# Performance work log

Hardware: AMD Instinct MI355X
Metric: run time of the kernel (lower is better)

The kernel has to match this reference:

```python
import jax, jax.numpy as jnp
import numpy as np

EPS = 1e-5
HEADS = 16
DIM_HEAD = 64
ROPE_THETA = 10000.0


def layer_norm(x, g, b):
    mu = x.mean(-1, keepdims=True)
    var = x.var(-1, keepdims=True)
    return (x - mu) / jnp.sqrt(var + EPS) * g + b


def apply_rope(t):
    # t: [b, h, n, d]; interleaved-pair RoPE (rotary-embedding-torch default)
    n, d = t.shape[-2], t.shape[-1]
    inv_freq = 1.0 / (ROPE_THETA ** (jnp.arange(0, d, 2, dtype=jnp.float32) / d))  # [d/2]
    freqs = jnp.arange(n, dtype=jnp.float32)[:, None] * inv_freq[None, :]          # [n, d/2]
    freqs = jnp.repeat(freqs, 2, axis=-1)                                          # [n, d]
    cos, sin = jnp.cos(freqs).astype(t.dtype), jnp.sin(freqs).astype(t.dtype)
    t2 = t.reshape(*t.shape[:-1], d // 2, 2)
    t_rot = jnp.stack((-t2[..., 1], t2[..., 0]), axis=-1).reshape(t.shape)
    return t * cos + t_rot * sin


def setup_inputs() -> dict:
    key = jax.random.key(0)
    k0, k1, k2 = jax.random.split(key, 3)
    B, N, D = 1, 4096, 1024
    inner = HEADS * DIM_HEAD
    x = jax.random.normal(k0, (B, N, D), jnp.float32)
    w_qkv = jax.random.normal(k1, (D, inner * 3), jnp.float32) * (D ** -0.5)
    w_out = jax.random.normal(k2, (inner, D), jnp.float32) * (inner ** -0.5)
    ln_g = jnp.ones((D,), jnp.float32)
    ln_b = jnp.zeros((D,), jnp.float32)
    return {"x": x, "w_qkv": w_qkv, "w_out": w_out, "ln_g": ln_g, "ln_b": ln_b}


def reference(x, w_qkv, w_out, ln_g, ln_b):
    B, N, D = x.shape
    H, DH = HEADS, DIM_HEAD
    scale = DH ** -0.5

    h = layer_norm(x, ln_g, ln_b)
    qkv = h @ w_qkv                                    # [b, n, 3*inner]
    q, k, v = jnp.split(qkv, 3, axis=-1)
    to_heads = lambda t: t.reshape(B, N, H, DH).transpose(0, 2, 1, 3)  # [b,h,n,d]
    q, k, v = to_heads(q), to_heads(k), to_heads(v)

    new_k, new_v = k, v  # cache holds pre-RoPE k, v (as in original)

    q = apply_rope(q)
    k = apply_rope(k)

    dots = jnp.einsum('bhid,bhjd->bhij', q, k) * scale  # [b,h,n,n]
    causal_mask = jnp.triu(jnp.ones((N, N), dtype=bool), 1)
    dots = jnp.where(causal_mask, -jnp.inf, dots)
    attn = jax.nn.softmax(dots, axis=-1)
    out = jnp.einsum('bhij,bhjd->bhid', attn, v)        # [b,h,n,d]
    out = out.transpose(0, 2, 1, 3).reshape(B, N, H * DH)
    return out @ w_out, new_k, new_v
```

## Files before the change

kernel.cpp:

```cpp
#include <hip/hip_runtime.h>
#include <math.h>

#define D_MODEL 1024
#define N_SEQ   4096
#define N_HEADS 16
#define DHEAD   64
#define QKV_COLS 3072

typedef short bf16x8 __attribute__((ext_vector_type(8)));
typedef short bf16x4 __attribute__((ext_vector_type(4)));
typedef float f32x4  __attribute__((ext_vector_type(4)));

#define MFMA32(a, b, c) __builtin_amdgcn_mfma_f32_16x16x32_bf16(a, b, c, 0, 0, 0)
#define MFMA16(a, b, c) __builtin_amdgcn_mfma_f32_16x16x16bf16_1k(a, b, c, 0, 0, 0)

static __device__ __forceinline__ unsigned short f2bf(float f) {
    union { float f; unsigned u; } v; v.f = f;
    unsigned r = (v.u + 0x7fffu + ((v.u >> 16) & 1u)) >> 16;
    return (unsigned short)r;
}

static __device__ __forceinline__ bf16x4 pack_bf16x4(float a, float b, float c, float d) {
    union { float f; unsigned u; } x0, x1, x2, x3;
    x0.f = a; x1.f = b; x2.f = c; x3.f = d;
    union { unsigned u[2]; bf16x4 v; } r;
    r.u[0] = __builtin_amdgcn_perm(x1.u, x0.u, 0x07060302u);
    r.u[1] = __builtin_amdgcn_perm(x3.u, x2.u, 0x07060302u);
    return r.v;
}

typedef __attribute__((address_space(1))) const void* gas_t;
typedef __attribute__((address_space(3))) void* las_t;
static __device__ __forceinline__ void load_lds16(const unsigned short* g, unsigned short* l) {
    __builtin_amdgcn_global_load_lds((gas_t)g, (las_t)l, 16, 0, 0);
}

__global__ __launch_bounds__(256) void ln_kernel(const float* __restrict__ x,
                                                 const float* __restrict__ g,
                                                 const float* __restrict__ b,
                                                 unsigned short* __restrict__ h) {
    int row = blockIdx.x;
    int t = threadIdx.x;
    float4 v = ((const float4*)(x + (size_t)row * D_MODEL))[t];
    float s  = v.x + v.y + v.z + v.w;
    float ss = v.x*v.x + v.y*v.y + v.z*v.z + v.w*v.w;
    for (int off = 32; off; off >>= 1) {
        s  += __shfl_down(s, off);
        ss += __shfl_down(ss, off);
    }
    __shared__ float sm[4], ssm[4];
    __shared__ float mu_s, rs_s;
    int wave = t >> 6, lane = t & 63;
    if (lane == 0) { sm[wave] = s; ssm[wave] = ss; }
    __syncthreads();
    if (t == 0) {
        float S = 0.f, SS = 0.f;
        for (int w = 0; w < 4; w++) { S += sm[w]; SS += ssm[w]; }
        float mu = S / D_MODEL;
        float var = SS / D_MODEL - mu * mu;
        mu_s = mu;
        rs_s = rsqrtf(var + 1e-5f);
    }
    __syncthreads();
    float mu = mu_s, rs = rs_s;
    float4 gv = ((const float4*)g)[t];
    float4 bv = ((const float4*)b)[t];
    ushort4 o;
    o.x = f2bf((v.x - mu) * rs * gv.x + bv.x);
    o.y = f2bf((v.y - mu) * rs * gv.y + bv.y);
    o.z = f2bf((v.z - mu) * rs * gv.z + bv.z);
    o.w = f2bf((v.w - mu) * rs * gv.w + bv.w);
    *(ushort4*)(h + (size_t)row * D_MODEL + t * 4) = o;
}

__global__ __launch_bounds__(256) void transpose_cvt(const float* __restrict__ W,
                                                     unsigned short* __restrict__ Wt,
                                                     int K, int N) {
    __shared__ float tile[64][65];
    int k0 = blockIdx.x * 64, n0 = blockIdx.y * 64;
    int t = threadIdx.x;
#pragma unroll
    for (int p = 0; p < 16; p++) {
        int idx = p * 256 + t;
        int r = idx >> 6, c = idx & 63;
        tile[r][c] = W[(size_t)(k0 + r) * N + n0 + c];
    }
    __syncthreads();
#pragma unroll
    for (int p = 0; p < 16; p++) {
        int idx = p * 256 + t;
        int r2 = idx >> 6, c2 = idx & 63;
        Wt[(size_t)(n0 + r2) * K + k0 + c2] = f2bf(tile[c2][r2]);
    }
}

__global__ __launch_bounds__(256) void gemm_bt128(const unsigned short* __restrict__ A,
                                                  const unsigned short* __restrict__ Bt,
                                                  float* __restrict__ C,
                                                  int M, int N, int K) {
    __shared__ unsigned short As[128 * 32];
    __shared__ unsigned short Bs[128 * 32];
    int t = threadIdx.x;
    int w = t >> 6, lane = t & 63;
    int l16 = lane & 15, quad = lane >> 4;
    int wr = w >> 1, wc = w & 1;
    int m0 = blockIdx.x * 128, n0 = blockIdx.y * 128;
    int srow = lane >> 2, scol = (lane & 3) * 8;
    int c0 = w * 2, c1 = c0 + 1;

    f32x4 acc[4][4] = {};

    for (int k0 = 0; k0 < K; k0 += 32) {
        __syncthreads();
        load_lds16(A  + (size_t)(m0 + c0 * 16 + srow) * K + k0 + scol, &As[c0 * 512 + lane * 8]);
        load_lds16(A  + (size_t)(m0 + c1 * 16 + srow) * K + k0 + scol, &As[c1 * 512 + lane * 8]);
        load_lds16(Bt + (size_t)(n0 + c0 * 16 + srow) * K + k0 + scol, &Bs[c0 * 512 + lane * 8]);
        load_lds16(Bt + (size_t)(n0 + c1 * 16 + srow) * K + k0 + scol, &Bs[c1 * 512 + lane * 8]);
        __syncthreads();
        bf16x8 a[4], b[4];
#pragma unroll
        for (int mt = 0; mt < 4; mt++)
            a[mt] = *(const bf16x8*)&As[(wr * 64 + mt * 16 + l16) * 32 + quad * 8];
#pragma unroll
        for (int nt = 0; nt < 4; nt++)
            b[nt] = *(const bf16x8*)&Bs[(wc * 64 + nt * 16 + l16) * 32 + quad * 8];
#pragma unroll
        for (int mt = 0; mt < 4; mt++)
#pragma unroll
            for (int nt = 0; nt < 4; nt++)
                acc[mt][nt] = MFMA32(a[mt], b[nt], acc[mt][nt]);
    }
#pragma unroll
    for (int mt = 0; mt < 4; mt++)
#pragma unroll
        for (int nt = 0; nt < 4; nt++)
#pragma unroll
            for (int r = 0; r < 4; r++)
                C[(size_t)(m0 + wr * 64 + mt * 16 + quad * 4 + r) * N + n0 + wc * 64 + nt * 16 + l16] =
                    acc[mt][nt][r];
}

__global__ __launch_bounds__(256) void rope_cache_kernel(const float* __restrict__ qkv,
                                                         float* __restrict__ out_k,
                                                         float* __restrict__ out_v,
                                                         unsigned short* __restrict__ q_bf,
                                                         unsigned short* __restrict__ k_bf,
                                                         unsigned short* __restrict__ vt_bf) {
    __shared__ unsigned short Vt[64 * 72];
    int nt = blockIdx.x, h = blockIdx.y;
    int n0 = nt * 64;
    int t = threadIdx.x;
    int row = t >> 2;
    int n = n0 + row;
    const float* src = qkv + (size_t)n * QKV_COLS + h * 64;
    size_t nd_base = ((size_t)h * N_SEQ + n) * 64;
#pragma unroll
    for (int j = 0; j < 4; j++) {
        int c = (t & 3) * 4 + j * 16;
        float4 q4 = *(const float4*)(src + c);
        float4 k4 = *(const float4*)(src + 1024 + c);
        float4 v4 = *(const float4*)(src + 2048 + c);
        *(float4*)(out_k + nd_base + c) = k4;
        *(float4*)(out_v + nd_base + c) = v4;
        float i0 = (float)(c >> 1), i1 = i0 + 1.f;
        float if0 = powf(10000.0f, -i0 / 32.0f);
        float if1 = powf(10000.0f, -i1 / 32.0f);
        float s0, c0s, s1, c1s;
        sincosf((float)n * if0, &s0, &c0s);
        sincosf((float)n * if1, &s1, &c1s);
        ushort4 qo, ko;
        qo.x = f2bf(q4.x * c0s - q4.y * s0); qo.y = f2bf(q4.y * c0s + q4.x * s0);
        qo.z = f2bf(q4.z * c1s - q4.w * s1); qo.w = f2bf(q4.w * c1s + q4.z * s1);
        ko.x = f2bf(k4.x * c0s - k4.y * s0); ko.y = f2bf(k4.y * c0s + k4.x * s0);
        ko.z = f2bf(k4.z * c1s - k4.w * s1); ko.w = f2bf(k4.w * c1s + k4.z * s1);
        *(ushort4*)(q_bf + nd_base + c) = qo;
        *(ushort4*)(k_bf + nd_base + c) = ko;
        ushort4 vo;
        vo.x = f2bf(v4.x); vo.y = f2bf(v4.y); vo.z = f2bf(v4.z); vo.w = f2bf(v4.w);
        *(ushort4*)&Vt[row * 72 + c] = vo;
    }
    __syncthreads();
    int d = t >> 2;
    int nb = (t & 3) * 16;
    unsigned short tmp[16];
#pragma unroll
    for (int i = 0; i < 16; i++) tmp[i] = Vt[(nb + i) * 72 + d];
    unsigned short* dst = vt_bf + ((size_t)h * DHEAD + d) * N_SEQ + n0 + nb;
#pragma unroll
    for (int i = 0; i < 16; i++) dst[i] = tmp[i];
}

__global__ __launch_bounds__(256, 4) void flash_mfma(const unsigned short* __restrict__ q_bf,
                                                     const unsigned short* __restrict__ k_bf,
                                                     const unsigned short* __restrict__ vt_bf,
                                                     unsigned short* __restrict__ attn_bf,
                                                     float* __restrict__ part_O,
                                                     float* __restrict__ part_l) {
    int idx = blockIdx.x;
    int h = idx & 15;
    int u = idx >> 4;
    int Qt, cc;
    bool partial = (u < 72);
    if (partial) {
        int r = 71 - u;
        if (r < 16)      { Qt = 8 + (r >> 1); cc = r & 1; }
        else if (r < 40) { int q3 = r - 16; int d3 = q3 / 3; Qt = 16 + d3; cc = q3 - 3 * d3; }
        else             { int q4 = r - 40; Qt = 24 + (q4 >> 2); cc = q4 & 3; }
    } else { Qt = 79 - u; cc = 0; }
    int kt0 = cc * 16;
    int kt_end = min(kt0 + 15, 2 * Qt + 1);

    int t = threadIdx.x;
    int w = t >> 6, lane = t & 63;
    int l16 = lane & 15, quad = lane >> 4;
    int sw = l16 & 7;

    __shared__ unsigned short Ks[64 * 64];
    __shared__ unsigned short Vs[64 * 64];

    int qr0 = Qt * 128 + w * 32;
    const unsigned short* Kg = k_bf + (size_t)h * N_SEQ * DHEAD;
    const unsigned short* Vg = vt_bf + (size_t)h * DHEAD * N_SEQ;

    bf16x8 bq[2][2];
#pragma unroll
    for (int qg = 0; qg < 2; qg++) {
        const unsigned short* qp = q_bf + ((size_t)h * N_SEQ + qr0 + qg * 16 + l16) * 64 + quad * 8;
        bq[qg][0] = *(const bf16x8*)(qp);
        bq[qg][1] = *(const bf16x8*)(qp + 32);
    }
    f32x4 O[2][4] = {};
    float lp[2] = {0.f, 0.f};
    int my_kmax = (qr0 + 31) >> 6;

    int srow = t >> 3;
    int scol = ((t & 7) ^ (srow & 7)) * 8;
    const float CEXP = 0.18033688011112042f;

    for (int kt = kt0; kt <= kt_end; kt++) {
        int k0 = kt << 6;
        __syncthreads();
        load_lds16(Kg + (size_t)(k0 + srow) * 64 + scol,         &Ks[t * 8]);
        load_lds16(Kg + (size_t)(k0 + srow + 32) * 64 + scol,    &Ks[t * 8 + 2048]);
        load_lds16(Vg + (size_t)srow * N_SEQ + k0 + scol,        &Vs[t * 8]);
        load_lds16(Vg + (size_t)(srow + 32) * N_SEQ + k0 + scol, &Vs[t * 8 + 2048]);
        __syncthreads();
        if (kt > my_kmax) continue;

        bf16x4 pf[2][4];
#pragma unroll
        for (int tt = 0; tt < 4; tt++) {
            int kbase = k0 + tt * 16;
            bf16x4 pz = (bf16x4){0, 0, 0, 0};
            if (kbase >= qr0 + 32) { pf[0][tt] = pz; pf[1][tt] = pz; continue; }
            int krow = tt * 16 + l16;
            bf16x8 kf0 = *(const bf16x8*)&Ks[krow * 64 + ((quad ^ sw) * 8)];
            bf16x8 kf1 = *(const bf16x8*)&Ks[krow * 64 + (((quad + 4) ^ sw) * 8)];
#pragma unroll
            for (int qg = 0; qg < 2; qg++) {
                int qb = qr0 + qg * 16;
                if (kbase > qb) { pf[qg][tt] = pz; continue; }
                f32x4 s = (f32x4){0.f, 0.f, 0.f, 0.f};
                s = MFMA32(kf0, bq[qg][0], s);
                s = MFMA32(kf1, bq[qg][1], s);
                float p0 = exp2f(s[0] * CEXP);
                float p1 = exp2f(s[1] * CEXP);
                float p2 = exp2f(s[2] * CEXP);
                float p3 = exp2f(s[3] * CEXP);
                if (kbase == qb) {
                    if (quad * 4 + 0 > l16) p0 = 0.f;
                    if (quad * 4 + 1 > l16) p1 = 0.f;
                    if (quad * 4 + 2 > l16) p2 = 0.f;
                    if (quad * 4 + 3 > l16) p3 = 0.f;
                }
                lp[qg] += (p0 + p1) + (p2 + p3);
                pf[qg][tt] = pack_bf16x4(p0, p1, p2, p3);
            }
        }
#pragma unroll
        for (int tt = 0; tt < 4; tt++) {
            if (k0 + tt * 16 < qr0 + 32) {
#pragma unroll
                for (int dt = 0; dt < 4; dt++) {
                    int vrow = dt * 16 + l16;
                    bf16x4 va = *(const bf16x4*)&Vs[vrow * 64 +
                                (((2 * tt + (quad >> 1)) ^ sw) * 8) + (quad & 1) * 4];
                    O[0][dt] = MFMA16(va, pf[0][tt], O[0][dt]);
                    O[1][dt] = MFMA16(va, pf[1][tt], O[1][dt]);
                }
            }
        }
    }

#pragma unroll
    for (int qg = 0; qg < 2; qg++) {
        float l = lp[qg];
        l += __shfl_xor(l, 16);
        l += __shfl_xor(l, 32);
        if (!partial) {
            float inv = 1.0f / l;
#pragma unroll
            for (int dt = 0; dt < 4; dt++) {
                ushort4 o;
                o.x = f2bf(O[qg][dt][0] * inv);
                o.y = f2bf(O[qg][dt][1] * inv);
                o.z = f2bf(O[qg][dt][2] * inv);
                o.w = f2bf(O[qg][dt][3] * inv);
                *(ushort4*)(attn_bf + (size_t)(qr0 + qg * 16 + l16) * D_MODEL + h * 64 + dt * 16 + quad * 4) = o;
            }
        } else {
            int uid = h * 72 + u;
            size_t ob = (size_t)uid * 8192;
            int qcol = w * 32 + qg * 16 + l16;
#pragma unroll
            for (int dt = 0; dt < 4; dt++)
#pragma unroll
                for (int r = 0; r < 4; r++)
                    part_O[ob + (size_t)(dt * 16 + quad * 4 + r) * 128 + qcol] = O[qg][dt][r];
            if (quad == 0) part_l[uid * 128 + qcol] = l;
        }
    }
}

__global__ __launch_bounds__(256) void combine_kernel(const float* __restrict__ part_O,
                                                      const float* __restrict__ part_l,
                                                      unsigned short* __restrict__ attn_bf) {
    int Qt = 8 + blockIdx.x;
    int h  = blockIdx.y;
    int nc = (Qt + 8) >> 3;
    int t = threadIdx.x;
    int q = t & 127;
    int dh = (t >> 7) * 32;
    float l = 0.f;
    float acc[32];
#pragma unroll
    for (int d = 0; d < 32; d++) acc[d] = 0.f;
    for (int c = 0; c < nc; c++) {
        int r;
        if (Qt < 16)      r = 2 * (Qt - 8) + c;
        else if (Qt < 24) r = 16 + 3 * (Qt - 16) + c;
        else              r = 40 + 4 * (Qt - 24) + c;
        int uid = h * 72 + (71 - r);
        l += part_l[uid * 128 + q];
        const float* po = part_O + (size_t)uid * 8192 + (size_t)dh * 128 + q;
#pragma unroll
        for (int d = 0; d < 32; d++) acc[d] += po[d * 128];
    }
    float inv = 1.0f / l;
    unsigned short* op = attn_bf + (size_t)(Qt * 128 + q) * D_MODEL + h * 64 + dh;
#pragma unroll
    for (int d = 0; d < 32; d++) op[d] = f2bf(acc[d] * inv);
}

extern "C" void kernel_launch(void* const* d_in, const int* in_sizes, int n_in,
                              void* d_out, int out_size, void* d_ws, size_t ws_size,
                              hipStream_t stream) {
    const float* x     = (const float*)d_in[0];
    const float* w_qkv = (const float*)d_in[1];
    const float* w_out = (const float*)d_in[2];
    const float* ln_g  = (const float*)d_in[3];
    const float* ln_b  = (const float*)d_in[4];

    float* out   = (float*)d_out;
    float* out_k = (float*)d_out + 4194304;
    float* out_v = (float*)d_out + 8388608;

    char* ws = (char*)d_ws;
    const size_t MiB = 1048576;
    float*          qkv_f   = (float*)(ws);
    unsigned short* h_bf    = (unsigned short*)(ws + 48*MiB);
    unsigned short* wqkvT   = (unsigned short*)(ws + 56*MiB);
    unsigned short* q_bf    = (unsigned short*)(ws + 48*MiB);
    unsigned short* k_bf    = (unsigned short*)(ws + 56*MiB);
    unsigned short* vt_bf   = (unsigned short*)(ws + 64*MiB);
    unsigned short* attn_bf = (unsigned short*)(ws);
    float*          part_l  = (float*)(ws + 8*MiB);
    float*          part_O  = (float*)(ws + 9*MiB);
    unsigned short* woutT   = (unsigned short*)(ws + 72*MiB);

    transpose_cvt<<<dim3(16, 48), 256, 0, stream>>>(w_qkv, wqkvT, D_MODEL, QKV_COLS);
    transpose_cvt<<<dim3(16, 16), 256, 0, stream>>>(w_out, woutT, D_MODEL, D_MODEL);
    ln_kernel<<<N_SEQ, 256, 0, stream>>>(x, ln_g, ln_b, h_bf);
    gemm_bt128<<<dim3(32, 24), 256, 0, stream>>>(h_bf, wqkvT, qkv_f, N_SEQ, QKV_COLS, D_MODEL);
    rope_cache_kernel<<<dim3(64, 16), 256, 0, stream>>>(qkv_f, out_k, out_v, q_bf, k_bf, vt_bf);
    flash_mfma<<<1280, 256, 0, stream>>>(q_bf, k_bf, vt_bf, attn_bf, part_O, part_l);
    combine_kernel<<<dim3(24, 16), 256, 0, stream>>>(part_O, part_l, attn_bf);
    gemm_bt128<<<dim3(32, 8), 256, 0, stream>>>(attn_bf, woutT, out, N_SEQ, D_MODEL, D_MODEL);
}
```

Baseline: 274.0 us.

## Fuse RoPE, cache writes and V transpose into QKV GEMM epilogue

The QKV GEMM now writes its outputs directly in their final forms: fp32 k/v cache, bf16 RoPE'd K, bf16 transposed V, and bf16 Q pre-multiplied by the softmax scale. This removes the fp32 qkv intermediate round trip and the separate rope kernel. Q RoPE is moved into the flash kernel's Q load, and split-K partial outputs are stored as bf16 instead of fp32 to halve that traffic. The costs are scattered 2-byte epilogue stores with a poor coalescing pattern, and extra rounding of Q and the partials to bf16.

```diff
diff --git a/kernel.cpp b/kernel.cpp
--- a/kernel.cpp
+++ b/kernel.cpp
@@ -14,18 +14,25 @@
 #define MFMA32(a, b, c) __builtin_amdgcn_mfma_f32_16x16x32_bf16(a, b, c, 0, 0, 0)
 #define MFMA16(a, b, c) __builtin_amdgcn_mfma_f32_16x16x16bf16_1k(a, b, c, 0, 0, 0)
 
+#define QSCALE  0.18033688011112042f
+#define NLOG2TH 0.41524101186092029f
+
 static __device__ __forceinline__ unsigned short f2bf(float f) {
     union { float f; unsigned u; } v; v.f = f;
     unsigned r = (v.u + 0x7fffu + ((v.u >> 16) & 1u)) >> 16;
     return (unsigned short)r;
 }
-
+static __device__ __forceinline__ float bf2f(unsigned short u) {
+    union { unsigned u; float f; } v; v.u = ((unsigned)u) << 16; return v.f;
+}
+static __device__ __forceinline__ unsigned packbf2(float a, float b) {
+    union { float f; unsigned u; } x0, x1; x0.f = a; x1.f = b;
+    return __builtin_amdgcn_perm(x1.u, x0.u, 0x07060302u);
+}
 static __device__ __forceinline__ bf16x4 pack_bf16x4(float a, float b, float c, float d) {
-    union { float f; unsigned u; } x0, x1, x2, x3;
-    x0.f = a; x1.f = b; x2.f = c; x3.f = d;
     union { unsigned u[2]; bf16x4 v; } r;
-    r.u[0] = __builtin_amdgcn_perm(x1.u, x0.u, 0x07060302u);
-    r.u[1] = __builtin_amdgcn_perm(x3.u, x2.u, 0x07060302u);
+    r.u[0] = packbf2(a, b);
+    r.u[1] = packbf2(c, d);
     return r.v;
 }
 
@@ -140,61 +147,112 @@
                     acc[mt][nt][r];
 }
 
-__global__ __launch_bounds__(256) void rope_cache_kernel(const float* __restrict__ qkv,
-                                                         float* __restrict__ out_k,
-                                                         float* __restrict__ out_v,
-                                                         unsigned short* __restrict__ q_bf,
-                                                         unsigned short* __restrict__ k_bf,
-                                                         unsigned short* __restrict__ vt_bf) {
-    __shared__ unsigned short Vt[64 * 72];
-    int nt = blockIdx.x, h = blockIdx.y;
-    int n0 = nt * 64;
-    int t = threadIdx.x;
-    int row = t >> 2;
-    int n = n0 + row;
-    const float* src = qkv + (size_t)n * QKV_COLS + h * 64;
-    size_t nd_base = ((size_t)h * N_SEQ + n) * 64;
-#pragma unroll
-    for (int j = 0; j < 4; j++) {
-        int c = (t & 3) * 4 + j * 16;
-        float4 q4 = *(const float4*)(src + c);
-        float4 k4 = *(const float4*)(src + 1024 + c);
-        float4 v4 = *(const float4*)(src + 2048 + c);
-        *(float4*)(out_k + nd_base + c) = k4;
-        *(float4*)(out_v + nd_base + c) = v4;
-        float i0 = (float)(c >> 1), i1 = i0 + 1.f;
-        float if0 = powf(10000.0f, -i0 / 32.0f);
-        float if1 = powf(10000.0f, -i1 / 32.0f);
-        float s0, c0s, s1, c1s;
-        sincosf((float)n * if0, &s0, &c0s);
-        sincosf((float)n * if1, &s1, &c1s);
-        ushort4 qo, ko;
-        qo.x = f2bf(q4.x * c0s - q4.y * s0); qo.y = f2bf(q4.y * c0s + q4.x * s0);
-        qo.z = f2bf(q4.z * c1s - q4.w * s1); qo.w = f2bf(q4.w * c1s + q4.z * s1);
-        ko.x = f2bf(k4.x * c0s - k4.y * s0); ko.y = f2bf(k4.y * c0s + k4.x * s0);
-        ko.z = f2bf(k4.z * c1s - k4.w * s1); ko.w = f2bf(k4.w * c1s + k4.z * s1);
-        *(ushort4*)(q_bf + nd_base + c) = qo;
-        *(ushort4*)(k_bf + nd_base + c) = ko;
-        ushort4 vo;
-        vo.x = f2bf(v4.x); vo.y = f2bf(v4.y); vo.z = f2bf(v4.z); vo.w = f2bf(v4.w);
-        *(ushort4*)&Vt[row * 72 + c] = vo;
-    }
-    __syncthreads();
-    int d = t >> 2;
-    int nb = (t & 3) * 16;
-    unsigned short tmp[16];
-#pragma unroll
-    for (int i = 0; i < 16; i++) tmp[i] = Vt[(nb + i) * 72 + d];
-    unsigned short* dst = vt_bf + ((size_t)h * DHEAD + d) * N_SEQ + n0 + nb;
-#pragma unroll
-    for (int i = 0; i < 16; i++) dst[i] = tmp[i];
+__global__ __launch_bounds__(256) void gemm_qkv_fused(const unsigned short* __restrict__ A,
+                                                      const unsigned short* __restrict__ Bt,
+                                                      float* __restrict__ out_k,
+                                                      float* __restrict__ out_v,
+                                                      unsigned short* __restrict__ q_bf,
+                                                      unsigned short* __restrict__ k_bf,
+                                                      unsigned short* __restrict__ vt_bf) {
+    const int K = D_MODEL, N = QKV_COLS;
+    __shared__ unsigned short As[128 * 32];
+    __shared__ unsigned short Bs[128 * 32];
+    int t = threadIdx.x;
+    int w = t >> 6, lane = t & 63;
+    int l16 = lane & 15, quad = lane >> 4;
+    int wr = w >> 1, wc = w & 1;
+    int by = blockIdx.y;
+    int m0 = blockIdx.x * 128, n0 = by * 128;
+    int srow = lane >> 2, scol = (lane & 3) * 8;
+    int c0 = w * 2, c1 = c0 + 1;
+
+    f32x4 acc[4][4] = {};
+
+    for (int k0 = 0; k0 < K; k0 += 32) {
+        __syncthreads();
+        load_lds16(A  + (size_t)(m0 + c0 * 16 + srow) * K + k0 + scol, &As[c0 * 512 + lane * 8]);
+        load_lds16(A  + (size_t)(m0 + c1 * 16 + srow) * K + k0 + scol, &As[c1 * 512 + lane * 8]);
+        load_lds16(Bt + (size_t)(n0 + c0 * 16 + srow) * K + k0 + scol, &Bs[c0 * 512 + lane * 8]);
+        load_lds16(Bt + (size_t)(n0 + c1 * 16 + srow) * K + k0 + scol, &Bs[c1 * 512 + lane * 8]);
+        __syncthreads();
+        bf16x8 a[4], b[4];
+#pragma unroll
+        for (int mt = 0; mt < 4; mt++)
+            a[mt] = *(const bf16x8*)&As[(wr * 64 + mt * 16 + l16) * 32 + quad * 8];
+#pragma unroll
+        for (int nt = 0; nt < 4; nt++)
+            b[nt] = *(const bf16x8*)&Bs[(wc * 64 + nt * 16 + l16) * 32 + quad * 8];
+#pragma unroll
+        for (int mt = 0; mt < 4; mt++)
+#pragma unroll
+            for (int nt = 0; nt < 4; nt++)
+                acc[mt][nt] = MFMA32(a[mt], b[nt], acc[mt][nt]);
+    }
+
+    int typ = by >> 3;
+    int hh  = (by & 7) * 2 + wc;
+    int nbase = m0 + wr * 64;
+
+    if (typ == 0) {
+#pragma unroll
+        for (int mt = 0; mt < 4; mt++)
+#pragma unroll
+            for (int nt = 0; nt < 4; nt++) {
+                int d = nt * 16 + l16;
+#pragma unroll
+                for (int r = 0; r < 4; r++) {
+                    int n = nbase + mt * 16 + quad * 4 + r;
+                    q_bf[((size_t)hh * N_SEQ + n) * 64 + d] = f2bf(acc[mt][nt][r] * QSCALE);
+                }
+            }
+    } else if (typ == 1) {
+        float f_nt[4];
+#pragma unroll
+        for (int nt = 0; nt < 4; nt++)
+            f_nt[nt] = exp2f((float)((nt * 16 + l16) >> 1) * -NLOG2TH);
+#pragma unroll
+        for (int mt = 0; mt < 4; mt++)
+#pragma unroll
+            for (int nt = 0; nt < 4; nt++) {
+                int d = nt * 16 + l16;
+#pragma unroll
+                for (int r = 0; r < 4; r++) {
+                    int n = nbase + mt * 16 + quad * 4 + r;
+                    float x = acc[mt][nt][r];
+                    out_k[((size_t)hh * N_SEQ + n) * 64 + d] = x;
+                    float p = __shfl_xor(x, 1);
+                    float sv, cv;
+                    sincosf((float)n * f_nt[nt], &sv, &cv);
+                    float ro = (d & 1) ? (x * cv + p * sv) : (x * cv - p * sv);
+                    k_bf[((size_t)hh * N_SEQ + n) * 64 + d] = f2bf(ro);
+                }
+            }
+    } else {
+#pragma unroll
+        for (int mt = 0; mt < 4; mt++)
+#pragma unroll
+            for (int nt = 0; nt < 4; nt++) {
+                int d = nt * 16 + l16;
+#pragma unroll
+                for (int r = 0; r < 4; r++) {
+                    int n = nbase + mt * 16 + quad * 4 + r;
+                    out_v[((size_t)hh * N_SEQ + n) * 64 + d] = acc[mt][nt][r];
+                }
+                ushort4 o;
+                o.x = f2bf(acc[mt][nt][0]);
+                o.y = f2bf(acc[mt][nt][1]);
+                o.z = f2bf(acc[mt][nt][2]);
+                o.w = f2bf(acc[mt][nt][3]);
+                *(ushort4*)&vt_bf[((size_t)hh * DHEAD + d) * N_SEQ + nbase + mt * 16 + quad * 4] = o;
+            }
+    }
 }
 
 __global__ __launch_bounds__(256, 4) void flash_mfma(const unsigned short* __restrict__ q_bf,
                                                      const unsigned short* __restrict__ k_bf,
                                                      const unsigned short* __restrict__ vt_bf,
                                                      unsigned short* __restrict__ attn_bf,
-                                                     float* __restrict__ part_O,
+                                                     unsigned short* __restrict__ part_O,
                                                      float* __restrict__ part_l) {
     int idx = blockIdx.x;
     int h = idx & 15;
@@ -225,9 +283,23 @@
     bf16x8 bq[2][2];
 #pragma unroll
     for (int qg = 0; qg < 2; qg++) {
+        float nf = (float)(qr0 + qg * 16 + l16);
         const unsigned short* qp = q_bf + ((size_t)h * N_SEQ + qr0 + qg * 16 + l16) * 64 + quad * 8;
-        bq[qg][0] = *(const bf16x8*)(qp);
-        bq[qg][1] = *(const bf16x8*)(qp + 32);
+#pragma unroll
+        for (int c = 0; c < 2; c++) {
+            bf16x8 raw = *(const bf16x8*)(qp + c * 32);
+            union { unsigned u[4]; bf16x8 v; } pk;
+#pragma unroll
+            for (int m = 0; m < 4; m++) {
+                float x0 = bf2f((unsigned short)raw[2 * m]);
+                float x1 = bf2f((unsigned short)raw[2 * m + 1]);
+                float fi = exp2f((float)(quad * 4 + c * 16 + m) * -NLOG2TH);
+                float sv, cv;
+                sincosf(nf * fi, &sv, &cv);
+                pk.u[m] = packbf2(x0 * cv - x1 * sv, x1 * cv + x0 * sv);
+            }
+            bq[qg][c] = pk.v;
+        }
     }
     f32x4 O[2][4] = {};
     float lp[2] = {0.f, 0.f};
@@ -235,7 +307,6 @@
 
     int srow = t >> 3;
     int scol = ((t & 7) ^ (srow & 7)) * 8;
-    const float CEXP = 0.18033688011112042f;
 
     for (int kt = kt0; kt <= kt_end; kt++) {
         int k0 = kt << 6;
@@ -263,10 +334,10 @@
                 f32x4 s = (f32x4){0.f, 0.f, 0.f, 0.f};
                 s = MFMA32(kf0, bq[qg][0], s);
                 s = MFMA32(kf1, bq[qg][1], s);
-                float p0 = exp2f(s[0] * CEXP);
-                float p1 = exp2f(s[1] * CEXP);
-                float p2 = exp2f(s[2] * CEXP);
-                float p3 = exp2f(s[3] * CEXP);
+                float p0 = exp2f(s[0]);
+                float p1 = exp2f(s[1]);
+                float p2 = exp2f(s[2]);
+                float p3 = exp2f(s[3]);
                 if (kbase == qb) {
                     if (quad * 4 + 0 > l16) p0 = 0.f;
                     if (quad * 4 + 1 > l16) p1 = 0.f;
@@ -316,13 +387,13 @@
             for (int dt = 0; dt < 4; dt++)
 #pragma unroll
                 for (int r = 0; r < 4; r++)
-                    part_O[ob + (size_t)(dt * 16 + quad * 4 + r) * 128 + qcol] = O[qg][dt][r];
+                    part_O[ob + (size_t)(dt * 16 + quad * 4 + r) * 128 + qcol] = f2bf(O[qg][dt][r]);
             if (quad == 0) part_l[uid * 128 + qcol] = l;
         }
     }
 }
 
-__global__ __launch_bounds__(256) void combine_kernel(const float* __restrict__ part_O,
+__global__ __launch_bounds__(256) void combine_kernel(const unsigned short* __restrict__ part_O,
                                                       const float* __restrict__ part_l,
                                                       unsigned short* __restrict__ attn_bf) {
     int Qt = 8 + blockIdx.x;
@@ -342,9 +413,9 @@
         else              r = 40 + 4 * (Qt - 24) + c;
         int uid = h * 72 + (71 - r);
         l += part_l[uid * 128 + q];
-        const float* po = part_O + (size_t)uid * 8192 + (size_t)dh * 128 + q;
-#pragma unroll
-        for (int d = 0; d < 32; d++) acc[d] += po[d * 128];
+        const unsigned short* po = part_O + (size_t)uid * 8192 + (size_t)dh * 128 + q;
+#pragma unroll
+        for (int d = 0; d < 32; d++) acc[d] += bf2f(po[d * 128]);
     }
     float inv = 1.0f / l;
     unsigned short* op = attn_bf + (size_t)(Qt * 128 + q) * D_MODEL + h * 64 + dh;
@@ -367,22 +438,20 @@
 
     char* ws = (char*)d_ws;
     const size_t MiB = 1048576;
-    float*          qkv_f   = (float*)(ws);
-    unsigned short* h_bf    = (unsigned short*)(ws + 48*MiB);
-    unsigned short* wqkvT   = (unsigned short*)(ws + 56*MiB);
-    unsigned short* q_bf    = (unsigned short*)(ws + 48*MiB);
-    unsigned short* k_bf    = (unsigned short*)(ws + 56*MiB);
-    unsigned short* vt_bf   = (unsigned short*)(ws + 64*MiB);
-    unsigned short* attn_bf = (unsigned short*)(ws);
-    float*          part_l  = (float*)(ws + 8*MiB);
-    float*          part_O  = (float*)(ws + 9*MiB);
-    unsigned short* woutT   = (unsigned short*)(ws + 72*MiB);
+    unsigned short* q_bf    = (unsigned short*)(ws);
+    unsigned short* k_bf    = (unsigned short*)(ws + 8*MiB);
+    unsigned short* vt_bf   = (unsigned short*)(ws + 16*MiB);
+    unsigned short* attn_bf = (unsigned short*)(ws + 24*MiB);
+    float*          part_l  = (float*)(ws + 32*MiB);
+    unsigned short* part_O  = (unsigned short*)(ws + 33*MiB);
+    unsigned short* h_bf    = (unsigned short*)(ws + 52*MiB);
+    unsigned short* wqkvT   = (unsigned short*)(ws + 60*MiB);
+    unsigned short* woutT   = (unsigned short*)(ws + 66*MiB);
 
     transpose_cvt<<<dim3(16, 48), 256, 0, stream>>>(w_qkv, wqkvT, D_MODEL, QKV_COLS);
     transpose_cvt<<<dim3(16, 16), 256, 0, stream>>>(w_out, woutT, D_MODEL, D_MODEL);
     ln_kernel<<<N_SEQ, 256, 0, stream>>>(x, ln_g, ln_b, h_bf);
-    gemm_bt128<<<dim3(32, 24), 256, 0, stream>>>(h_bf, wqkvT, qkv_f, N_SEQ, QKV_COLS, D_MODEL);
-    rope_cache_kernel<<<dim3(64, 16), 256, 0, stream>>>(qkv_f, out_k, out_v, q_bf, k_bf, vt_bf);
+    gemm_qkv_fused<<<dim3(32, 24), 256, 0, stream>>>(h_bf, wqkvT, out_k, out_v, q_bf, k_bf, vt_bf);
     flash_mfma<<<1280, 256, 0, stream>>>(q_bf, k_bf, vt_bf, attn_bf, part_O, part_l);
     combine_kernel<<<dim3(24, 16), 256, 0, stream>>>(part_O, part_l, attn_bf);
     gemm_bt128<<<dim3(32, 8), 256, 0, stream>>>(attn_bf, woutT, out, N_SEQ, D_MODEL, D_MODEL);
```

After: 592.3 us. +116.2%, slower.
